# Optimization experiments

Hardware: AMD Instinct MI355X
Metric: run time of the kernel (lower is better)

## Reference

```python
import jax, jax.numpy as jnp
import numpy as np

NEG_SLOPE = 0.2
EPS = 1e-16  # PyG softmax denominator epsilon


def setup_inputs() -> dict:
    key = jax.random.key(0)
    k1, k2, k3, k4 = jax.random.split(key, 4)
    N, E, F_in, F_out = 50000, 800000, 256, 128
    x = jax.random.normal(k1, (N, F_in), dtype=jnp.float32)
    edge_index = jax.random.randint(k2, (2, E), 0, N, dtype=jnp.int64)
    # Glorot-ish scaled params (values irrelevant to correctness, scale keeps softmax sane)
    W = jax.random.normal(k3, (F_in, F_out), dtype=jnp.float32) * (1.0 / np.sqrt(F_in))
    ka, kb = jax.random.split(k4)
    att_src = jax.random.normal(ka, (F_out,), dtype=jnp.float32) * (1.0 / np.sqrt(F_out))
    att_dst = jax.random.normal(kb, (F_out,), dtype=jnp.float32) * (1.0 / np.sqrt(F_out))
    bias = jnp.zeros((F_out,), dtype=jnp.float32)
    return {"x": x, "edge_index": edge_index, "W": W, "att_src": att_src, "att_dst": att_dst, "bias": bias}


def reference(x, edge_index, W, att_src, att_dst, bias):
    N = x.shape[0]
    # Linear transform (no bias in PyG GATConv's lin)
    h = x @ W  # [N, F_out]
    # Add self loops (GATConv default add_self_loops=True)
    loops = jnp.arange(N, dtype=edge_index.dtype)
    src = jnp.concatenate([edge_index[0], loops])  # [E+N]
    dst = jnp.concatenate([edge_index[1], loops])
    # Per-node attention logits, gathered per edge
    a_src = h @ att_src  # [N]
    a_dst = h @ att_dst  # [N]
    e = jax.nn.leaky_relu(a_src[src] + a_dst[dst], NEG_SLOPE)  # [E+N]
    # Segment softmax over incoming edges of each destination node
    e_max = jax.ops.segment_max(e, dst, num_segments=N)  # every segment nonempty (self loops)
    e_exp = jnp.exp(e - e_max[dst])
    denom = jax.ops.segment_sum(e_exp, dst, num_segments=N)
    alpha = e_exp / (denom[dst] + EPS)  # [E+N]
    # Scatter-aggregate weighted source features
    out = jax.ops.segment_sum(alpha[:, None] * h[src], dst, num_segments=N)  # [N, F_out]
    return out + bias
```

## Files before the change

kernel.cpp:

```cpp
#include <hip/hip_runtime.h>
#include <cstdint>
#include <cstddef>

#define F_IN 256
#define F_OUT 128
#define NEG_SLOPE 0.2f
#define NPB 64
#define MAXBUK 1024
#define BCAP 2048
#define EPB 4096
#define WT_STRIDE 72

typedef short short8 __attribute__((ext_vector_type(8)));
typedef float f32x4 __attribute__((ext_vector_type(4)));

__device__ __forceinline__ unsigned short f2bf_rne(float f) {
  unsigned u = __float_as_uint(f);
  u += 0x7FFFu + ((u >> 16) & 1u);
  return (unsigned short)(u >> 16);
}

__device__ __forceinline__ unsigned cvt_pk_bf16(float lo, float hi) {
  unsigned r;
  asm volatile("v_cvt_pk_bf16_f32 %0, %1, %2" : "=v"(r) : "v"(lo), "v"(hi));
  return r;
}

__device__ __forceinline__ float bf_lo(unsigned u) { return __uint_as_float(u << 16); }
__device__ __forceinline__ float bf_hi(unsigned u) { return __uint_as_float(u & 0xFFFF0000u); }

__global__ __launch_bounds__(256) void setup_kernel(const float* __restrict__ W,
                                                    unsigned short* __restrict__ Wt,
                                                    int* __restrict__ bucketcnt, int nbuk) {
  int idx = blockIdx.x * 256 + threadIdx.x;
  if (idx < F_IN * F_OUT) {
    int n = idx & 127, k = idx >> 7;
    Wt[(size_t)n * F_IN + k] = f2bf_rne(W[(size_t)k * F_OUT + n]);
  }
  if (idx < nbuk) bucketcnt[idx] = 0;
}

__global__ __launch_bounds__(256, 4) void gemm_build_kernel(
    const float* __restrict__ x, const unsigned short* __restrict__ Wt,
    const float* __restrict__ att_src, const float* __restrict__ att_dst,
    unsigned short* __restrict__ hb, float* __restrict__ a_src, float* __restrict__ a_dst,
    int N, const int* __restrict__ ei, int* __restrict__ bucketcnt,
    unsigned* __restrict__ csrw, int E, int nbuk, int buildBlocks) {
  __shared__ __attribute__((aligned(16))) char lds_raw[128 * WT_STRIDE * 2];
  const int tid = threadIdx.x;

  if ((int)blockIdx.x < buildBlocks) {
    int* lhist = (int*)lds_raw;
    int* gbase = (int*)(lds_raw + 4096);
    const int e0 = blockIdx.x * EPB;
    for (int i = tid; i < nbuk; i += 256) lhist[i] = 0;
    __syncthreads();
    int lr[16], lb[16];
    unsigned lw[16];
#pragma unroll
    for (int i = 0; i < 16; ++i) {
      int e = e0 + i * 256 + tid;
      lb[i] = -1;
      if (e < E) {
        int s = ei[e], d = ei[E + e];
        lb[i] = d >> 6;
        lw[i] = ((unsigned)(d & 63) << 26) | (unsigned)s;
        lr[i] = atomicAdd(&lhist[lb[i]], 1);
      }
    }
    __syncthreads();
    for (int i = tid; i < nbuk; i += 256) {
      int c = lhist[i];
      if (c > 0) gbase[i] = atomicAdd(&bucketcnt[i], c);
    }
    __syncthreads();
#pragma unroll
    for (int i = 0; i < 16; ++i) {
      if (lb[i] >= 0) {
        int off = gbase[lb[i]] + lr[i];
        if (off < BCAP) csrw[(size_t)lb[i] * BCAP + off] = lw[i];
      }
    }
    return;
  }

  unsigned short* wt_l = (unsigned short*)lds_raw;
  const int bid  = blockIdx.x - buildBlocks;
  const int lane = tid & 63;
  const int wv   = tid >> 6;
  const int q    = lane >> 4;
  const int l16  = lane & 15;
  const int m0   = bid * 64;
  const int m    = m0 + wv * 16 + l16;
  const int mc   = (m < N) ? m : (N - 1);

  f32x4 acc[8];
#pragma unroll
  for (int i = 0; i < 8; ++i) acc[i] = (f32x4)(0.f);

  const int srow  = tid >> 1;
  const int shalf = tid & 1;

#pragma unroll 1
  for (int t = 0; t < 4; ++t) {
    {
      const unsigned short* g = Wt + (size_t)srow * F_IN + t * 64 + shalf * 32;
      unsigned short* l = wt_l + srow * WT_STRIDE + shalf * 32;
#pragma unroll
      for (int j = 0; j < 4; ++j)
        *(uint4*)(l + j * 8) = *(const uint4*)(g + j * 8);
    }
    __syncthreads();

#pragma unroll
    for (int s = 0; s < 2; ++s) {
      const int kg = t * 64 + s * 32 + q * 8;
      f32x4 a0 = *(const f32x4*)(x + (size_t)mc * F_IN + kg);
      f32x4 a1 = *(const f32x4*)(x + (size_t)mc * F_IN + kg + 4);
      union { short8 s8; unsigned u[4]; } cvt;
      cvt.u[0] = cvt_pk_bf16(a0[0], a0[1]);
      cvt.u[1] = cvt_pk_bf16(a0[2], a0[3]);
      cvt.u[2] = cvt_pk_bf16(a1[0], a1[1]);
      cvt.u[3] = cvt_pk_bf16(a1[2], a1[3]);
      short8 av = cvt.s8;
#pragma unroll
      for (int nt = 0; nt < 8; ++nt) {
        short8 bv = *(const short8*)(wt_l + (nt * 16 + l16) * WT_STRIDE + s * 32 + q * 8);
        acc[nt] = __builtin_amdgcn_mfma_f32_16x16x32_bf16(av, bv, acc[nt], 0, 0, 0);
      }
    }
    __syncthreads();
  }

  float as_c[8], ad_c[8];
#pragma unroll
  for (int nt = 0; nt < 8; ++nt) {
    as_c[nt] = att_src[nt * 16 + l16];
    ad_c[nt] = att_dst[nt * 16 + l16];
  }
  float ps[4] = {0.f, 0.f, 0.f, 0.f}, pd[4] = {0.f, 0.f, 0.f, 0.f};
#pragma unroll
  for (int nt = 0; nt < 8; ++nt)
#pragma unroll
    for (int r = 0; r < 4; ++r) {
      ps[r] += acc[nt][r] * as_c[nt];
      pd[r] += acc[nt][r] * ad_c[nt];
    }
#pragma unroll
  for (int r = 0; r < 4; ++r) {
    int gm = m0 + wv * 16 + q * 4 + r;
    if (gm < N) {
#pragma unroll
      for (int nt = 0; nt < 8; ++nt)
        hb[(size_t)gm * F_OUT + nt * 16 + l16] = f2bf_rne(acc[nt][r]);
    }
  }
#pragma unroll
  for (int r = 0; r < 4; ++r) {
#pragma unroll
    for (int off = 1; off <= 8; off <<= 1) {
      ps[r] += __shfl_xor(ps[r], off, 64);
      pd[r] += __shfl_xor(pd[r], off, 64);
    }
  }
  if (l16 == 0) {
#pragma unroll
    for (int r = 0; r < 4; ++r) {
      int gm = m0 + wv * 16 + q * 4 + r;
      if (gm < N) { a_src[gm] = ps[r]; a_dst[gm] = pd[r]; }
    }
  }
}

__global__ __launch_bounds__(256) void aggregate_kernel(const unsigned short* __restrict__ hb,
                                                        const unsigned* __restrict__ csrw,
                                                        const float* __restrict__ a_src,
                                                        const float* __restrict__ a_dst,
                                                        const int* __restrict__ bucketcnt,
                                                        const float* __restrict__ bias,
                                                        float* __restrict__ out, int N) {
  __shared__ unsigned sw[BCAP];
  __shared__ unsigned sorted[BCAP + NPB];
  __shared__ int start[NPB + 1];
  __shared__ int fill[NPB];
  __shared__ float adl[NPB];
  const int tid = threadIdx.x;
  const int n0  = blockIdx.x * NPB;
  int cnt = bucketcnt[blockIdx.x];
  cnt = (cnt < BCAP) ? cnt : BCAP;

  if (tid < NPB) {
    int n = n0 + tid;
    start[1 + tid] = (n < N) ? 1 : 0;
    fill[tid] = 1;
    adl[tid] = (n < N) ? a_dst[n] : 0.f;
  }
  __syncthreads();
  for (int j = tid; j < cnt; j += 256) {
    unsigned w = csrw[(size_t)blockIdx.x * BCAP + j];
    sw[j] = w;
    atomicAdd(&start[1 + (int)(w >> 26)], 1);
  }
  __syncthreads();
  if (tid < NPB) {
    int incl = start[1 + tid];
#pragma unroll
    for (int off = 1; off < NPB; off <<= 1) {
      int t = __shfl_up(incl, off, 64);
      if (tid >= off) incl += t;
    }
    start[1 + tid] = incl;
    if (tid == 0) start[0] = 0;
  }
  __syncthreads();
  if (tid < NPB && n0 + tid < N)
    sorted[start[tid]] = ((unsigned)tid << 26) | (unsigned)(n0 + tid);
  for (int j = tid; j < cnt; j += 256) {
    unsigned w = sw[j];
    int loc = (int)(w >> 26);
    sorted[start[loc] + atomicAdd(&fill[loc], 1)] = w;
  }
  __syncthreads();

  const int g   = tid >> 4;
  const int l16 = tid & 15;
  const unsigned short* hrow = hb + l16 * 8;
  const float4 bb0 = *(const float4*)(bias + l16 * 8);
  const float4 bb1 = *(const float4*)(bias + l16 * 8 + 4);
#pragma unroll 1
  for (int r = 0; r < 4; ++r) {
    int loc = g + r * 16;
    int n = n0 + loc;
    if (n >= N) continue;
    int b0 = start[loc], b1 = start[loc + 1];
    f32x4 acc0 = (f32x4)(0.f), acc1 = (f32x4)(0.f);
    float s = 0.f;
    for (int jb = b0; jb < b1; jb += 8) {
      int jj = jb + (l16 & 7);
      float p = 0.f;
      int c = 0;
      if (jj < b1) {
        unsigned w = sorted[jj];
        c = (int)(w & 0x03FFFFFFu);
        float e = a_src[c] + adl[loc];
        e = (e > 0.f) ? e : NEG_SLOPE * e;
        p = __expf(e);
      }
      s += (l16 < 8) ? p : 0.f;
#pragma unroll
      for (int k = 0; k < 8; ++k) {
        float pk = __shfl(p, k, 8);
        int   ck = __shfl(c, k, 8);
        const uint4 hv = *(const uint4*)(hrow + (size_t)ck * F_OUT);
        acc0[0] += pk * bf_lo(hv.x); acc0[1] += pk * bf_hi(hv.x);
        acc0[2] += pk * bf_lo(hv.y); acc0[3] += pk * bf_hi(hv.y);
        acc1[0] += pk * bf_lo(hv.z); acc1[1] += pk * bf_hi(hv.z);
        acc1[2] += pk * bf_lo(hv.w); acc1[3] += pk * bf_hi(hv.w);
      }
    }
#pragma unroll
    for (int off = 1; off < 16; off <<= 1) s += __shfl_xor(s, off, 16);

    float sc = 1.f / (s + 1e-16f);
    float4 o0, o1;
    o0.x = acc0[0] * sc + bb0.x;
    o0.y = acc0[1] * sc + bb0.y;
    o0.z = acc0[2] * sc + bb0.z;
    o0.w = acc0[3] * sc + bb0.w;
    o1.x = acc1[0] * sc + bb1.x;
    o1.y = acc1[1] * sc + bb1.y;
    o1.z = acc1[2] * sc + bb1.z;
    o1.w = acc1[3] * sc + bb1.w;
    *(float4*)&out[(size_t)n * F_OUT + l16 * 8]     = o0;
    *(float4*)&out[(size_t)n * F_OUT + l16 * 8 + 4] = o1;
  }
}

extern "C" void kernel_launch(void* const* d_in, const int* in_sizes, int n_in,
                              void* d_out, int out_size, void* d_ws, size_t ws_size,
                              hipStream_t stream) {
  const float* x     = (const float*)d_in[0];
  const int*   ei    = (const int*)d_in[1];
  const float* W     = (const float*)d_in[2];
  const float* att_s = (const float*)d_in[3];
  const float* att_d = (const float*)d_in[4];
  const float* bias  = (const float*)d_in[5];
  float* out = (float*)d_out;

  const int N = in_sizes[0] / F_IN;
  const int E = in_sizes[1] / 2;
  const int nbuk = (N + NPB - 1) / NPB;
  const int gemmBlocks  = (N + 63) / 64;
  const int buildBlocks = (E + EPB - 1) / EPB;

  char* p = (char*)d_ws;
  unsigned short* wt = (unsigned short*)p; p += (size_t)F_IN * F_OUT * sizeof(unsigned short);
  unsigned short* hb = (unsigned short*)p; p += (size_t)N * F_OUT * sizeof(unsigned short);
  float* a_src = (float*)p;  p += (size_t)N * sizeof(float);
  float* a_dst = (float*)p;  p += (size_t)N * sizeof(float);
  int*   bcnt  = (int*)p;    p += (size_t)nbuk * sizeof(int);
  p = (char*)(((uintptr_t)p + 15) & ~(uintptr_t)15);
  unsigned* csrw = (unsigned*)p; p += (size_t)nbuk * BCAP * sizeof(unsigned);

  int setup_n = (F_IN * F_OUT > nbuk) ? F_IN * F_OUT : nbuk;
  setup_kernel<<<(setup_n + 255) / 256, 256, 0, stream>>>(W, wt, bcnt, nbuk);
  gemm_build_kernel<<<buildBlocks + gemmBlocks, 256, 0, stream>>>(
      x, wt, att_s, att_d, hb, a_src, a_dst, N, ei, bcnt, csrw, E, nbuk, buildBlocks);
  aggregate_kernel<<<nbuk, 256, 0, stream>>>(hb, csrw, a_src, a_dst, bcnt, bias, out, N);
}
```

Baseline: 149.9 us.

## Process 128 rows per GEMM block and halve edges per build block

```diff
diff --git a/kernel.cpp b/kernel.cpp
--- a/kernel.cpp
+++ b/kernel.cpp
@@ -8,7 +8,7 @@
 #define NPB 64
 #define MAXBUK 1024
 #define BCAP 2048
-#define EPB 4096
+#define EPB 2048
 #define WT_STRIDE 72
 
 typedef short short8 __attribute__((ext_vector_type(8)));
@@ -55,10 +55,10 @@
     const int e0 = blockIdx.x * EPB;
     for (int i = tid; i < nbuk; i += 256) lhist[i] = 0;
     __syncthreads();
-    int lr[16], lb[16];
-    unsigned lw[16];
-#pragma unroll
-    for (int i = 0; i < 16; ++i) {
+    int lr[8], lb[8];
+    unsigned lw[8];
+#pragma unroll
+    for (int i = 0; i < 8; ++i) {
       int e = e0 + i * 256 + tid;
       lb[i] = -1;
       if (e < E) {
@@ -75,7 +75,7 @@
     }
     __syncthreads();
 #pragma unroll
-    for (int i = 0; i < 16; ++i) {
+    for (int i = 0; i < 8; ++i) {
       if (lb[i] >= 0) {
         int off = gbase[lb[i]] + lr[i];
         if (off < BCAP) csrw[(size_t)lb[i] * BCAP + off] = lw[i];
@@ -90,13 +90,15 @@
   const int wv   = tid >> 6;
   const int q    = lane >> 4;
   const int l16  = lane & 15;
-  const int m0   = bid * 64;
-  const int m    = m0 + wv * 16 + l16;
-  const int mc   = (m < N) ? m : (N - 1);
-
-  f32x4 acc[8];
-#pragma unroll
-  for (int i = 0; i < 8; ++i) acc[i] = (f32x4)(0.f);
+  const int m0   = bid * 128;
+  const int mA   = m0 + wv * 16 + l16;
+  const int mB   = mA + 64;
+  const int mcA  = (mA < N) ? mA : (N - 1);
+  const int mcB  = (mB < N) ? mB : (N - 1);
+
+  f32x4 accA[8], accB[8];
+#pragma unroll
+  for (int i = 0; i < 8; ++i) { accA[i] = (f32x4)(0.f); accB[i] = (f32x4)(0.f); }
 
   const int srow  = tid >> 1;
   const int shalf = tid & 1;
@@ -115,18 +117,25 @@
 #pragma unroll
     for (int s = 0; s < 2; ++s) {
       const int kg = t * 64 + s * 32 + q * 8;
-      f32x4 a0 = *(const f32x4*)(x + (size_t)mc * F_IN + kg);
-      f32x4 a1 = *(const f32x4*)(x + (size_t)mc * F_IN + kg + 4);
-      union { short8 s8; unsigned u[4]; } cvt;
-      cvt.u[0] = cvt_pk_bf16(a0[0], a0[1]);
-      cvt.u[1] = cvt_pk_bf16(a0[2], a0[3]);
-      cvt.u[2] = cvt_pk_bf16(a1[0], a1[1]);
-      cvt.u[3] = cvt_pk_bf16(a1[2], a1[3]);
-      short8 av = cvt.s8;
+      f32x4 a0 = *(const f32x4*)(x + (size_t)mcA * F_IN + kg);
+      f32x4 a1 = *(const f32x4*)(x + (size_t)mcA * F_IN + kg + 4);
+      f32x4 b0 = *(const f32x4*)(x + (size_t)mcB * F_IN + kg);
+      f32x4 b1 = *(const f32x4*)(x + (size_t)mcB * F_IN + kg + 4);
+      union { short8 s8; unsigned u[4]; } ca, cb;
+      ca.u[0] = cvt_pk_bf16(a0[0], a0[1]);
+      ca.u[1] = cvt_pk_bf16(a0[2], a0[3]);
+      ca.u[2] = cvt_pk_bf16(a1[0], a1[1]);
+      ca.u[3] = cvt_pk_bf16(a1[2], a1[3]);
+      cb.u[0] = cvt_pk_bf16(b0[0], b0[1]);
+      cb.u[1] = cvt_pk_bf16(b0[2], b0[3]);
+      cb.u[2] = cvt_pk_bf16(b1[0], b1[1]);
+      cb.u[3] = cvt_pk_bf16(b1[2], b1[3]);
+      short8 avA = ca.s8, avB = cb.s8;
 #pragma unroll
       for (int nt = 0; nt < 8; ++nt) {
         short8 bv = *(const short8*)(wt_l + (nt * 16 + l16) * WT_STRIDE + s * 32 + q * 8);
-        acc[nt] = __builtin_amdgcn_mfma_f32_16x16x32_bf16(av, bv, acc[nt], 0, 0, 0);
+        accA[nt] = __builtin_amdgcn_mfma_f32_16x16x32_bf16(avA, bv, accA[nt], 0, 0, 0);
+        accB[nt] = __builtin_amdgcn_mfma_f32_16x16x32_bf16(avB, bv, accB[nt], 0, 0, 0);
       }
     }
     __syncthreads();
@@ -138,36 +147,49 @@
     as_c[nt] = att_src[nt * 16 + l16];
     ad_c[nt] = att_dst[nt * 16 + l16];
   }
-  float ps[4] = {0.f, 0.f, 0.f, 0.f}, pd[4] = {0.f, 0.f, 0.f, 0.f};
+  float psA[4] = {0, 0, 0, 0}, pdA[4] = {0, 0, 0, 0};
+  float psB[4] = {0, 0, 0, 0}, pdB[4] = {0, 0, 0, 0};
 #pragma unroll
   for (int nt = 0; nt < 8; ++nt)
 #pragma unroll
     for (int r = 0; r < 4; ++r) {
-      ps[r] += acc[nt][r] * as_c[nt];
-      pd[r] += acc[nt][r] * ad_c[nt];
+      psA[r] += accA[nt][r] * as_c[nt];
+      pdA[r] += accA[nt][r] * ad_c[nt];
+      psB[r] += accB[nt][r] * as_c[nt];
+      pdB[r] += accB[nt][r] * ad_c[nt];
     }
 #pragma unroll
   for (int r = 0; r < 4; ++r) {
-    int gm = m0 + wv * 16 + q * 4 + r;
-    if (gm < N) {
+    int gmA = m0 + wv * 16 + q * 4 + r;
+    int gmB = gmA + 64;
+    if (gmA < N) {
 #pragma unroll
       for (int nt = 0; nt < 8; ++nt)
-        hb[(size_t)gm * F_OUT + nt * 16 + l16] = f2bf_rne(acc[nt][r]);
+        hb[(size_t)gmA * F_OUT + nt * 16 + l16] = f2bf_rne(accA[nt][r]);
+    }
+    if (gmB < N) {
+#pragma unroll
+      for (int nt = 0; nt < 8; ++nt)
+        hb[(size_t)gmB * F_OUT + nt * 16 + l16] = f2bf_rne(accB[nt][r]);
     }
   }
 #pragma unroll
   for (int r = 0; r < 4; ++r) {
 #pragma unroll
     for (int off = 1; off <= 8; off <<= 1) {
-      ps[r] += __shfl_xor(ps[r], off, 64);
-      pd[r] += __shfl_xor(pd[r], off, 64);
+      psA[r] += __shfl_xor(psA[r], off, 64);
+      pdA[r] += __shfl_xor(pdA[r], off, 64);
+      psB[r] += __shfl_xor(psB[r], off, 64);
+      pdB[r] += __shfl_xor(pdB[r], off, 64);
     }
   }
   if (l16 == 0) {
 #pragma unroll
     for (int r = 0; r < 4; ++r) {
-      int gm = m0 + wv * 16 + q * 4 + r;
-      if (gm < N) { a_src[gm] = ps[r]; a_dst[gm] = pd[r]; }
+      int gmA = m0 + wv * 16 + q * 4 + r;
+      int gmB = gmA + 64;
+      if (gmA < N) { a_src[gmA] = psA[r]; a_dst[gmA] = pdA[r]; }
+      if (gmB < N) { a_src[gmB] = psB[r]; a_dst[gmB] = pdB[r]; }
     }
   }
 }
@@ -290,7 +312,7 @@
   const int N = in_sizes[0] / F_IN;
   const int E = in_sizes[1] / 2;
   const int nbuk = (N + NPB - 1) / NPB;
-  const int gemmBlocks  = (N + 63) / 64;
+  const int gemmBlocks  = (N + 127) / 128;
   const int buildBlocks = (E + EPB - 1) / EPB;
 
   char* p = (char*)d_ws;
```

Result: slower. 163.4 us (+9.0%).
